# Performance work log

Measured on AMD Instinct MI355X. Metric: run time of the kernel, lower is better.

Reference implementation:

```python
import jax, jax.numpy as jnp
import numpy as np

N = 8192
F_IN, F1, F2 = 11, 16, 32
HEADS = 3
D_CAT = 2 * F2          # 64, concat of interface + neighborhood branches
D_POOL = D_CAT * HEADS  # 192


def setup_inputs() -> dict:
    key = jax.random.key(0)
    ks = jax.random.split(key, 16)
    s = 0.1
    return {
        "x_int": jax.random.normal(ks[0], (N, F_IN), jnp.float32),
        "x_nh": jax.random.normal(ks[1], (N, F_IN), jnp.float32),
        # dense soft adjacencies, scaled ~1/N so aggregates stay O(1)
        "adj_int": jax.random.uniform(ks[2], (N, N), jnp.float32) / N,
        "adj_nh": jax.random.uniform(ks[3], (N, N), jnp.float32) / N,
        "W1_int": jax.random.normal(ks[4], (F_IN, F1), jnp.float32) * s,
        "b1_int": jnp.zeros((F1,), jnp.float32),
        "W1_nh": jax.random.normal(ks[5], (F_IN, F1), jnp.float32) * s,
        "b1_nh": jnp.zeros((F1,), jnp.float32),
        "W2_int": jax.random.normal(ks[6], (F1, F2), jnp.float32) * s,
        "b2_int": jnp.zeros((F2,), jnp.float32),
        "W2_nh": jax.random.normal(ks[7], (F1, F2), jnp.float32) * s,
        "b2_nh": jnp.zeros((F2,), jnp.float32),
        "W_att": jax.random.normal(ks[8], (D_CAT, HEADS), jnp.float32) * s,
        "W_dense": jax.random.normal(ks[9], (D_POOL, 1), jnp.float32) * s,
        "b_dense": jnp.zeros((1,), jnp.float32),
    }


def _dgcn(A, x, W, b):
    # diffusion graph conv: aggregate neighbors then linear + relu
    return jax.nn.relu(A @ (x @ W) + b)


def reference(x_int, x_nh, adj_int, adj_nh,
              W1_int, b1_int, W1_nh, b1_nh,
              W2_int, b2_int, W2_nh, b2_nh,
              W_att, W_dense, b_dense):
    # conv1 / conv2, two parallel graph branches
    h_int = _dgcn(adj_int, x_int, W1_int, b1_int)   # [N, 16]
    h_nh = _dgcn(adj_nh, x_nh, W1_nh, b1_nh)        # [N, 16]
    h_int = _dgcn(adj_int, h_int, W2_int, b2_int)   # [N, 32]
    h_nh = _dgcn(adj_nh, h_nh, W2_nh, b2_nh)        # [N, 32]
    h = jnp.concatenate([h_int, h_nh], axis=1)      # [N, 64]
    # multi-head tanh self-attention pooling over nodes
    scores = jnp.tanh(h @ W_att)                    # [N, heads]
    att = jax.nn.softmax(scores, axis=0)            # softmax over nodes
    pooled = jnp.einsum('nh,nd->hd', att, h).reshape(1, D_POOL)  # [1, 192]
    out = pooled @ W_dense + b_dense                # [1, 1]
    return jnp.squeeze(out, 1)                      # [1]
```

## Files before the change

### kernel.cpp

```cpp
#include <hip/hip_runtime.h>


constexpr int N = 8192;

#define GLOBAL_AS __attribute__((address_space(1)))
#define LDS_AS __attribute__((address_space(3)))

__device__ __forceinline__ void gload_lds16(const float* g, float* l) {
    __builtin_amdgcn_global_load_lds((const GLOBAL_AS void*)g, (LDS_AS void*)l, 16, 0, 0);
}

__global__ void k_dense_in(const float* __restrict__ x0, const float* __restrict__ x1,
                           const float* __restrict__ W0, const float* __restrict__ W1,
                           float* __restrict__ o0, float* __restrict__ o1) {
    const int branch = blockIdx.y;
    const float* __restrict__ x = branch ? x1 : x0;
    const float* __restrict__ W = branch ? W1 : W0;
    float* __restrict__ o = branch ? o1 : o0;
    __shared__ float sW[11 * 16];
    if (threadIdx.x < 176) sW[threadIdx.x] = W[threadIdx.x];
    __syncthreads();
    const int n = blockIdx.x * blockDim.x + threadIdx.x;
    float xr[11];
#pragma unroll
    for (int j = 0; j < 11; ++j) xr[j] = x[n * 11 + j];
    float acc[16];
#pragma unroll
    for (int f = 0; f < 16; ++f) acc[f] = 0.f;
#pragma unroll
    for (int j = 0; j < 11; ++j)
#pragma unroll
        for (int f = 0; f < 16; ++f) acc[f] += xr[j] * sW[j * 16 + f];
#pragma unroll
    for (int q = 0; q < 4; ++q) {
        float4 r = make_float4(acc[q * 4 + 0], acc[q * 4 + 1], acc[q * 4 + 2], acc[q * 4 + 3]);
        *reinterpret_cast<float4*>(&o[n * 16 + q * 4]) = r;
    }
}

__global__ void k_dense_mid(const float* __restrict__ h0, const float* __restrict__ h1,
                            const float* __restrict__ W0, const float* __restrict__ W1,
                            float* __restrict__ o0, float* __restrict__ o1) {
    const int branch = blockIdx.y;
    const float* __restrict__ h = branch ? h1 : h0;
    const float* __restrict__ W = branch ? W1 : W0;
    float* __restrict__ o = branch ? o1 : o0;
    __shared__ float sW[16 * 32];
    for (int i = threadIdx.x; i < 512; i += blockDim.x) sW[i] = W[i];
    __syncthreads();
    const int n = blockIdx.x * blockDim.x + threadIdx.x;
    float hr[16];
#pragma unroll
    for (int q = 0; q < 4; ++q)
        *reinterpret_cast<float4*>(&hr[q * 4]) =
            *reinterpret_cast<const float4*>(&h[n * 16 + q * 4]);
    float acc[32];
#pragma unroll
    for (int f = 0; f < 32; ++f) acc[f] = 0.f;
#pragma unroll
    for (int j = 0; j < 16; ++j)
#pragma unroll
        for (int f = 0; f < 32; ++f) acc[f] += hr[j] * sW[j * 32 + f];
#pragma unroll
    for (int q = 0; q < 8; ++q) {
        float4 r = make_float4(acc[q * 4 + 0], acc[q * 4 + 1], acc[q * 4 + 2], acc[q * 4 + 3]);
        *reinterpret_cast<float4*>(&o[n * 32 + q * 4]) = r;
    }
}

template <int F>
__global__ __launch_bounds__(256, 2) void k_spmm(
    const float* __restrict__ A0, const float* __restrict__ A1,
    const float* __restrict__ Pm0, const float* __restrict__ Pm1,
    const float* __restrict__ b0, const float* __restrict__ b1,
    float* __restrict__ o0, float* __restrict__ o1, int ostride) {
    constexpr int TN = F / 4;
    constexpr int PJ = TN / 4;
    constexpr int KT = 256;
    const int branch = blockIdx.y;
    const float* __restrict__ A = branch ? A1 : A0;
    const float* __restrict__ Pm = branch ? Pm1 : Pm0;
    const float* __restrict__ bias = branch ? b1 : b0;
    float* __restrict__ o = branch ? o1 : o0;

    __shared__ float tile[2][32 * KT];

    const int lane = threadIdx.x & 63;
    const int wave = threadIdx.x >> 6;
    const int kg = lane & 15;
    const int cg = lane >> 4;
    const int c0 = cg * TN;
    const int row0 = blockIdx.x * 32;

    const float* gbase = A + (size_t)(row0 + wave * 8) * N + lane * 4;

    float acc[8][TN];
#pragma unroll
    for (int m = 0; m < 8; ++m)
#pragma unroll
        for (int j = 0; j < TN; ++j) acc[m][j] = 0.f;

    auto stage = [&](int buf, int K0) {
#pragma unroll
        for (int r = 0; r < 8; ++r)
            gload_lds16(gbase + (size_t)r * N + K0, &tile[buf][(wave * 8 + r) * KT]);
    };

    auto compute = [&](int buf, int K0) {
#pragma unroll
        for (int ks = 0; ks < 4; ++ks) {
            const int kk = ks * 64 + kg * 4;
            float4 p[4][PJ];
#pragma unroll
            for (int t = 0; t < 4; ++t)
#pragma unroll
                for (int j = 0; j < PJ; ++j)
                    p[t][j] = *reinterpret_cast<const float4*>(
                        Pm + (size_t)(K0 + kk + t) * F + c0 + j * 4);
#pragma unroll
            for (int m = 0; m < 8; ++m) {
                const float4 a = *reinterpret_cast<const float4*>(
                    &tile[buf][(wave * 8 + m) * KT + kk]);
#pragma unroll
                for (int t = 0; t < 4; ++t) {
                    const float av = (t == 0) ? a.x : (t == 1) ? a.y : (t == 2) ? a.z : a.w;
#pragma unroll
                    for (int j = 0; j < PJ; ++j) {
                        acc[m][j * 4 + 0] += av * p[t][j].x;
                        acc[m][j * 4 + 1] += av * p[t][j].y;
                        acc[m][j * 4 + 2] += av * p[t][j].z;
                        acc[m][j * 4 + 3] += av * p[t][j].w;
                    }
                }
            }
        }
    };

    stage(0, 0);
    __syncthreads();
    int cur = 0;
    for (int K0 = 0; K0 < N; K0 += KT) {
        if (K0 + KT < N) stage(cur ^ 1, K0 + KT);
        compute(cur, K0);
        __syncthreads();
        cur ^= 1;
    }

#pragma unroll
    for (int m = 0; m < 8; ++m)
#pragma unroll
        for (int j = 0; j < TN; ++j) {
            float v = acc[m][j];
            v += __shfl_xor(v, 1);
            v += __shfl_xor(v, 2);
            v += __shfl_xor(v, 4);
            v += __shfl_xor(v, 8);
            acc[m][j] = v;
        }
    if (kg == 0) {
#pragma unroll
        for (int m = 0; m < 8; ++m)
#pragma unroll
            for (int j = 0; j < PJ; ++j) {
                float4 r;
                r.x = fmaxf(acc[m][j * 4 + 0] + bias[c0 + j * 4 + 0], 0.f);
                r.y = fmaxf(acc[m][j * 4 + 1] + bias[c0 + j * 4 + 1], 0.f);
                r.z = fmaxf(acc[m][j * 4 + 2] + bias[c0 + j * 4 + 2], 0.f);
                r.w = fmaxf(acc[m][j * 4 + 3] + bias[c0 + j * 4 + 3], 0.f);
                *reinterpret_cast<float4*>(
                    &o[(size_t)(row0 + wave * 8 + m) * ostride + c0 + j * 4]) = r;
            }
    }
}

__global__ void k_att_pool(const float* __restrict__ h, const float* __restrict__ Watt,
                           const float* __restrict__ Wd, float* __restrict__ partials) {
    __shared__ float sWa[64 * 3];
    __shared__ float sWd[192];
    for (int i = threadIdx.x; i < 192; i += blockDim.x) {
        sWa[i] = Watt[i];
        sWd[i] = Wd[i];
    }
    __syncthreads();
    const int n = blockIdx.x * blockDim.x + threadIdx.x;
    float hv[64];
#pragma unroll
    for (int q = 0; q < 16; ++q)
        *reinterpret_cast<float4*>(&hv[q * 4]) =
            *reinterpret_cast<const float4*>(&h[(size_t)n * 64 + q * 4]);
    float s0 = 0.f, s1 = 0.f, s2 = 0.f;
#pragma unroll
    for (int d = 0; d < 64; ++d) {
        s0 += hv[d] * sWa[d * 3 + 0];
        s1 += hv[d] * sWa[d * 3 + 1];
        s2 += hv[d] * sWa[d * 3 + 2];
    }
    float dot0 = 0.f, dot1 = 0.f, dot2 = 0.f;
#pragma unroll
    for (int d = 0; d < 64; ++d) {
        dot0 += hv[d] * sWd[0 * 64 + d];
        dot1 += hv[d] * sWd[1 * 64 + d];
        dot2 += hv[d] * sWd[2 * 64 + d];
    }
    const float e0 = expf(tanhf(s0));
    const float e1 = expf(tanhf(s1));
    const float e2 = expf(tanhf(s2));
    float vals[6] = {e0, e1, e2, e0 * dot0, e1 * dot1, e2 * dot2};
#pragma unroll
    for (int i = 0; i < 6; ++i) {
        float v = vals[i];
#pragma unroll
        for (int off = 1; off < 64; off <<= 1) v += __shfl_xor(v, off);
        vals[i] = v;
    }
    __shared__ float sred[4][6];
    const int wave = threadIdx.x >> 6, lane = threadIdx.x & 63;
    if (lane == 0) {
#pragma unroll
        for (int i = 0; i < 6; ++i) sred[wave][i] = vals[i];
    }
    __syncthreads();
    if (threadIdx.x == 0) {
#pragma unroll
        for (int i = 0; i < 6; ++i)
            partials[blockIdx.x * 6 + i] = sred[0][i] + sred[1][i] + sred[2][i] + sred[3][i];
    }
}

__global__ void k_att_final(const float* __restrict__ partials, const float* __restrict__ bd,
                            float* __restrict__ out) {
    if (threadIdx.x == 0) {
        float Z0 = 0.f, Z1 = 0.f, Z2 = 0.f, U0 = 0.f, U1 = 0.f, U2 = 0.f;
        for (int b = 0; b < 32; ++b) {
            Z0 += partials[b * 6 + 0];
            Z1 += partials[b * 6 + 1];
            Z2 += partials[b * 6 + 2];
            U0 += partials[b * 6 + 3];
            U1 += partials[b * 6 + 4];
            U2 += partials[b * 6 + 5];
        }
        out[0] = U0 / Z0 + U1 / Z1 + U2 / Z2 + bd[0];
    }
}

extern "C" void kernel_launch(void* const* d_in, const int* in_sizes, int n_in,
                              void* d_out, int out_size, void* d_ws, size_t ws_size,
                              hipStream_t stream) {
    const float* x_int   = (const float*)d_in[0];
    const float* x_nh    = (const float*)d_in[1];
    const float* adj_int = (const float*)d_in[2];
    const float* adj_nh  = (const float*)d_in[3];
    const float* W1_int  = (const float*)d_in[4];
    const float* b1_int  = (const float*)d_in[5];
    const float* W1_nh   = (const float*)d_in[6];
    const float* b1_nh   = (const float*)d_in[7];
    const float* W2_int  = (const float*)d_in[8];
    const float* b2_int  = (const float*)d_in[9];
    const float* W2_nh   = (const float*)d_in[10];
    const float* b2_nh   = (const float*)d_in[11];
    const float* W_att   = (const float*)d_in[12];
    const float* W_dense = (const float*)d_in[13];
    const float* b_dense = (const float*)d_in[14];

    float* ws = (float*)d_ws;
    float* P1_0 = ws;
    float* P1_1 = ws + 131072;
    float* H1_0 = ws + 262144;
    float* H1_1 = ws + 393216;
    float* P2_0 = ws + 524288;
    float* P2_1 = ws + 786432;
    float* hcat = ws + 1048576;
    float* partials = ws + 1572864;
    float* out = (float*)d_out;

    k_dense_in<<<dim3(32, 2), 256, 0, stream>>>(x_int, x_nh, W1_int, W1_nh, P1_0, P1_1);
    k_spmm<16><<<dim3(256, 2), 256, 0, stream>>>(adj_int, adj_nh, P1_0, P1_1,
                                                 b1_int, b1_nh, H1_0, H1_1, 16);
    k_dense_mid<<<dim3(32, 2), 256, 0, stream>>>(H1_0, H1_1, W2_int, W2_nh, P2_0, P2_1);
    k_spmm<32><<<dim3(256, 2), 256, 0, stream>>>(adj_int, adj_nh, P2_0, P2_1,
                                                 b2_int, b2_nh, hcat, hcat + 32, 64);
    k_att_pool<<<32, 256, 0, stream>>>(hcat, W_att, W_dense, partials);
    k_att_final<<<1, 64, 0, stream>>>(partials, b_dense, out);
}
```

Baseline: 514.0 us.

## Restructure SpMM loop: hoist projection loads and drop block barriers

Reworks the dense-adjacency SpMM main loop. All projection-matrix rows for a K tile are now loaded into registers at the start of each iteration, ahead of issuing the next adjacency tile's global-to-LDS copy. The block-wide __syncthreads is replaced by an explicit per-wave vmcnt wait plus scheduling barriers. This is valid because each wave only stages and reads its own rows of the LDS tile. The aim is to cut barrier stalls and to overlap the streaming of the large adjacency matrix with FMA work, at the cost of many more live VGPRs for the hoisted projection values.

```diff
diff --git a/kernel.cpp b/kernel.cpp
--- a/kernel.cpp
+++ b/kernel.cpp
@@ -77,6 +77,7 @@
     constexpr int TN = F / 4;
     constexpr int PJ = TN / 4;
     constexpr int KT = 256;
+    constexpr int NT = N / KT;
     const int branch = blockIdx.y;
     const float* __restrict__ A = branch ? A1 : A0;
     const float* __restrict__ Pm = branch ? Pm1 : Pm0;
@@ -91,8 +92,13 @@
     const int cg = lane >> 4;
     const int c0 = cg * TN;
     const int row0 = blockIdx.x * 32;
-
-    const float* gbase = A + (size_t)(row0 + wave * 8) * N + lane * 4;
+    const float* gsrc = A + (size_t)(row0 + wave * 8) * N + lane * 4;
+
+    auto stage = [&](int buf, int K0) {
+#pragma unroll
+        for (int r = 0; r < 8; ++r)
+            gload_lds16(gsrc + (size_t)r * N + K0, &tile[buf][(wave * 8 + r) * KT]);
+    };
 
     float acc[8][TN];
 #pragma unroll
@@ -100,23 +106,28 @@
 #pragma unroll
         for (int j = 0; j < TN; ++j) acc[m][j] = 0.f;
 
-    auto stage = [&](int buf, int K0) {
-#pragma unroll
-        for (int r = 0; r < 8; ++r)
-            gload_lds16(gbase + (size_t)r * N + K0, &tile[buf][(wave * 8 + r) * KT]);
-    };
-
-    auto compute = [&](int buf, int K0) {
+    stage(0, 0);
+
+    for (int it = 0; it < NT; ++it) {
+        const int K0 = it * KT;
+        const int buf = it & 1;
+        asm volatile("s_waitcnt vmcnt(0)" ::: "memory");
+        __builtin_amdgcn_sched_barrier(0);
+        float4 p[4][4][PJ];
+#pragma unroll
+        for (int ks = 0; ks < 4; ++ks)
+#pragma unroll
+            for (int t = 0; t < 4; ++t)
+#pragma unroll
+                for (int j = 0; j < PJ; ++j)
+                    p[ks][t][j] = *reinterpret_cast<const float4*>(
+                        Pm + (size_t)(K0 + ks * 64 + kg * 4 + t) * F + c0 + j * 4);
+        __builtin_amdgcn_sched_barrier(0);
+        if (it + 1 < NT) stage(buf ^ 1, K0 + KT);
+        __builtin_amdgcn_sched_barrier(0);
 #pragma unroll
         for (int ks = 0; ks < 4; ++ks) {
             const int kk = ks * 64 + kg * 4;
-            float4 p[4][PJ];
-#pragma unroll
-            for (int t = 0; t < 4; ++t)
-#pragma unroll
-                for (int j = 0; j < PJ; ++j)
-                    p[t][j] = *reinterpret_cast<const float4*>(
-                        Pm + (size_t)(K0 + kk + t) * F + c0 + j * 4);
 #pragma unroll
             for (int m = 0; m < 8; ++m) {
                 const float4 a = *reinterpret_cast<const float4*>(
@@ -126,24 +137,14 @@
                     const float av = (t == 0) ? a.x : (t == 1) ? a.y : (t == 2) ? a.z : a.w;
 #pragma unroll
                     for (int j = 0; j < PJ; ++j) {
-                        acc[m][j * 4 + 0] += av * p[t][j].x;
-                        acc[m][j * 4 + 1] += av * p[t][j].y;
-                        acc[m][j * 4 + 2] += av * p[t][j].z;
-                        acc[m][j * 4 + 3] += av * p[t][j].w;
+                        acc[m][j * 4 + 0] += av * p[ks][t][j].x;
+                        acc[m][j * 4 + 1] += av * p[ks][t][j].y;
+                        acc[m][j * 4 + 2] += av * p[ks][t][j].z;
+                        acc[m][j * 4 + 3] += av * p[ks][t][j].w;
                     }
                 }
             }
         }
-    };
-
-    stage(0, 0);
-    __syncthreads();
-    int cur = 0;
-    for (int K0 = 0; K0 < N; K0 += KT) {
-        if (K0 + KT < N) stage(cur ^ 1, K0 + KT);
-        compute(cur, K0);
-        __syncthreads();
-        cur ^= 1;
     }
 
 #pragma unroll
```

Result: slower. 527.9 us (+2.7%).
